# Kernel tuning notes

Measured on AMD Instinct MI355X. Metric: run time of the kernel, lower is better.

The kernel has to match this reference:

```python
import jax, jax.numpy as jnp
import numpy as np

B, N, D = 8, 4096, 512      # batch, bag_size, model dim (in_dim == att_dim)
H, DH = 8, 64               # heads, dim_head
M = 256                     # landmarks (N % M == 0 -> no padding branch)
PINV_ITERS = 6
CONV_K = 33                 # residual depthwise conv kernel (lucidrains default)


def layernorm(x, g, b, eps=1e-5):
    mu = x.mean(-1, keepdims=True)
    var = ((x - mu) ** 2).mean(-1, keepdims=True)
    return (x - mu) * jax.lax.rsqrt(var + eps) * g + b


def moore_penrose_pinv(x, iters):
    # iterative Newton-Schulz pseudo-inverse, global max normalization as in lucidrains
    abs_x = jnp.abs(x)
    col = abs_x.sum(-1)
    row = abs_x.sum(-2)
    z = jnp.swapaxes(x, -1, -2) / (jnp.max(col) * jnp.max(row))
    I = jnp.eye(x.shape[-1], dtype=x.dtype)
    for _ in range(iters):
        xz = x @ z
        z = 0.25 * z @ (13.0 * I - xz @ (15.0 * I - xz @ (7.0 * I - xz)))
    return z


def setup_inputs() -> dict:
    key = jax.random.key(0)
    ks = jax.random.split(key, 12)
    s = 0.02
    return {
        "X": jax.random.normal(ks[0], (B, N, D), dtype=jnp.float32),
        "Wqkv": jax.random.normal(ks[1], (D, 3 * H * DH), dtype=jnp.float32) * s,
        "Wout": jax.random.normal(ks[2], (H * DH, D), dtype=jnp.float32) * s,
        "bout": jnp.zeros((D,), dtype=jnp.float32),
        "conv_w": jax.random.normal(ks[3], (H, 1, CONV_K, 1), dtype=jnp.float32) * s,
        "g1": jnp.ones((D,), dtype=jnp.float32),
        "beta1": jnp.zeros((D,), dtype=jnp.float32),
        "g2": jnp.ones((D,), dtype=jnp.float32),
        "beta2": jnp.zeros((D,), dtype=jnp.float32),
        "W1": jax.random.normal(ks[4], (D, 4 * D), dtype=jnp.float32) * s,
        "b1": jnp.zeros((4 * D,), dtype=jnp.float32),
        "W2": jax.random.normal(ks[5], (4 * D, D), dtype=jnp.float32) * s,
        "b2": jnp.zeros((D,), dtype=jnp.float32),
    }


def nystrom_attention(x, Wqkv, Wout, bout, conv_w):
    b, n, _ = x.shape
    qkv = x @ Wqkv                                   # (b, n, 3*H*DH)
    qkv = qkv.reshape(b, n, 3, H, DH)
    q = jnp.transpose(qkv[:, :, 0], (0, 2, 1, 3))    # (b, H, n, DH)
    k = jnp.transpose(qkv[:, :, 1], (0, 2, 1, 3))
    v = jnp.transpose(qkv[:, :, 2], (0, 2, 1, 3))
    q = q * (DH ** -0.5)

    l = n // M  # group size per landmark
    q_l = q.reshape(b, H, M, l, DH).mean(axis=3)     # (b, H, M, DH)
    k_l = k.reshape(b, H, M, l, DH).mean(axis=3)

    sim1 = jnp.einsum("bhnd,bhmd->bhnm", q, k_l)     # (b, H, n, M)
    sim2 = jnp.einsum("bhmd,bhld->bhml", q_l, k_l)   # (b, H, M, M)
    sim3 = jnp.einsum("bhmd,bhnd->bhmn", q_l, k)     # (b, H, M, n)

    attn1 = jax.nn.softmax(sim1, axis=-1)
    attn2 = jax.nn.softmax(sim2, axis=-1)
    attn3 = jax.nn.softmax(sim3, axis=-1)

    attn2_inv = moore_penrose_pinv(attn2, PINV_ITERS)
    out = (attn1 @ attn2_inv) @ (attn3 @ v)          # (b, H, n, DH)

    # residual depthwise conv over sequence dim, heads as channels
    res = jax.lax.conv_general_dilated(
        v, conv_w, window_strides=(1, 1),
        padding=((CONV_K // 2, CONV_K // 2), (0, 0)),
        dimension_numbers=("NCHW", "OIHW", "NCHW"),
        feature_group_count=H,
    )
    out = out + res

    out = jnp.transpose(out, (0, 2, 1, 3)).reshape(b, n, H * DH)
    return out @ Wout + bout


def reference(X, Wqkv, Wout, bout, conv_w, g1, beta1, g2, beta2, W1, b1, W2, b2):
    h = layernorm(X, g1, beta1)
    h = nystrom_attention(h, Wqkv, Wout, bout, conv_w)
    # MLP with residual (use_mlp=True); dropout=0.0 -> identity
    m = layernorm(h, g2, beta2)
    m = jax.nn.gelu(m @ W1 + b1, approximate=False) @ W2 + b2
    h = h + m
    # proj_out is Identity since out_dim == att_dim
    return h
```

## Files before the change

### kernel.cpp

```cpp
#include <hip/hip_runtime.h>
#include <hip/hip_bf16.h>
#include <cmath>

#define DEV __device__ __forceinline__

namespace {

constexpr int kB = 8, kN = 4096, kD = 512, kH = 8, kDH = 64, kM = 256, kL = 16, kCK = 33;
constexpr int kBN = kB * kN;
constexpr int kBH = kB * kH;
constexpr int kHD = kH * kDH;
constexpr int kD4 = 4 * kD;
constexpr int kQKVC = 3 * kHD;

typedef __attribute__((ext_vector_type(8))) short short8;
typedef __attribute__((ext_vector_type(4))) float f32x4;

DEV float toF(float x) { return x; }
DEV float toF(__hip_bfloat16 x) { return __bfloat162float(x); }
DEV __hip_bfloat16 f2b(float f) { return __float2bfloat16(f); }
DEV short f2s(float f) {
  __hip_bfloat16 h = __float2bfloat16(f);
  return *reinterpret_cast<short*>(&h);
}
DEV float us2f(unsigned short u) { return __uint_as_float((unsigned)u << 16); }
DEV unsigned short f2us(float f) {
  __hip_bfloat16 h = __float2bfloat16(f);
  return *reinterpret_cast<unsigned short*>(&h);
}
DEV float lo16(unsigned u) { return __uint_as_float(u << 16); }
DEV float hi16(unsigned u) { return __uint_as_float(u & 0xffff0000u); }

DEV float waveSum(float v) {
#pragma unroll
  for (int o = 32; o > 0; o >>= 1) v += __shfl_down(v, o, 64);
  return v;
}
DEV float waveMax(float v) {
#pragma unroll
  for (int o = 32; o > 0; o >>= 1) v = fmaxf(v, __shfl_down(v, o, 64));
  return v;
}
DEV float blockSum(float v, float* sb) {
  v = waveSum(v);
  int lane = threadIdx.x & 63, w = threadIdx.x >> 6;
  __syncthreads();
  if (lane == 0) sb[w] = v;
  __syncthreads();
  return sb[0] + sb[1] + sb[2] + sb[3];
}
DEV float blockMax(float v, float* sb) {
  v = waveMax(v);
  int lane = threadIdx.x & 63, w = threadIdx.x >> 6;
  __syncthreads();
  if (lane == 0) sb[w] = v;
  __syncthreads();
  return fmaxf(fmaxf(sb[0], sb[1]), fmaxf(sb[2], sb[3]));
}

__global__ __launch_bounds__(256) void detect_k(const unsigned* __restrict__ x,
                                                int* __restrict__ flag) {
  __shared__ int sc[4];
  int t = threadIdx.x;
  int cb = 0;
  for (int i = t; i < 4096; i += 256) {
    unsigned w = x[i];
    float b0 = __uint_as_float(w << 16);
    float b1 = __uint_as_float(w & 0xffff0000u);
    if (fabsf(b0) < 64.0f && (b0 == 0.0f || fabsf(b0) > 1e-20f)) cb++;
    if (fabsf(b1) < 64.0f && (b1 == 0.0f || fabsf(b1) > 1e-20f)) cb++;
  }
#pragma unroll
  for (int o = 32; o > 0; o >>= 1) cb += __shfl_down(cb, o, 64);
  if ((t & 63) == 0) sc[t >> 6] = cb;
  __syncthreads();
  if (t == 0) flag[0] = (sc[0] + sc[1] + sc[2] + sc[3] > 7373) ? 1 : 0;
}

__global__ void cvt_any_k(const void* __restrict__ s, float* __restrict__ d, int n,
                          const int* __restrict__ flag) {
  int i = blockIdx.x * 256 + threadIdx.x;
  if (i >= n) return;
  if (*flag)
    d[i] = toF(((const __hip_bfloat16*)s)[i]);
  else
    d[i] = ((const float*)s)[i];
}

__global__ void cvtT_k(const void* __restrict__ s, __hip_bfloat16* __restrict__ d, int K, int N,
                       const int* __restrict__ flag) {
  int i = blockIdx.x * 256 + threadIdx.x;
  if (i >= N * K) return;
  int n = i / K, k = i - n * K;
  float v = (*flag) ? toF(((const __hip_bfloat16*)s)[(long)k * N + n])
                    : ((const float*)s)[(long)k * N + n];
  d[i] = f2b(v);
}

__global__ void f32tob16_k(const float* __restrict__ s, __hip_bfloat16* __restrict__ d, int n) {
  int i = blockIdx.x * 256 + threadIdx.x;
  if (i < n) d[i] = f2b(s[i]);
}


__global__ __launch_bounds__(256) void ln1_k(const void* __restrict__ xv,
                                             const float* __restrict__ g,
                                             const float* __restrict__ be,
                                             __hip_bfloat16* __restrict__ o,
                                             const int* __restrict__ flag) {
  __shared__ float sb[4];
  size_t row = blockIdx.x;
  __hip_bfloat16* po = o + row * kD;
  int t = threadIdx.x;
  float v0, v1;
  if (*flag) {
    const __hip_bfloat16* pr = (const __hip_bfloat16*)xv + row * kD;
    v0 = toF(pr[t]);
    v1 = toF(pr[t + 256]);
  } else {
    const float* pr = (const float*)xv + row * kD;
    v0 = pr[t];
    v1 = pr[t + 256];
  }
  float s = blockSum(v0 + v1, sb);
  float ss = blockSum(v0 * v0 + v1 * v1, sb);
  float mu = s * (1.0f / kD);
  float var = ss * (1.0f / kD) - mu * mu;
  float rs = rsqrtf(var + 1e-5f);
  po[t] = f2b((v0 - mu) * rs * g[t] + be[t]);
  po[t + 256] = f2b((v1 - mu) * rs * g[t + 256] + be[t + 256]);
}

__global__ __launch_bounds__(256) void ln2stats_k(const float* __restrict__ x,
                                                  float* __restrict__ st) {
  __shared__ float sb[4];
  size_t row = blockIdx.x;
  const float* pr = x + row * kD;
  int t = threadIdx.x;
  float v0 = pr[t], v1 = pr[t + 256];
  float s = blockSum(v0 + v1, sb);
  float ss = blockSum(v0 * v0 + v1 * v1, sb);
  if (t == 0) {
    float mu = s * (1.0f / kD);
    float var = ss * (1.0f / kD) - mu * mu;
    st[2 * row] = mu;
    st[2 * row + 1] = rsqrtf(var + 1e-5f);
  }
}


__global__ void landmark_k(const __hip_bfloat16* __restrict__ src, float* __restrict__ dst) {
  int i = blockIdx.x * 256 + threadIdx.x;
  if (i >= kBH * kM * kDH) return;
  int dh = i & 63, m = (i >> 6) & 255, bh = i >> 14;
  const __hip_bfloat16* p = src + ((size_t)bh * kN + m * kL) * kDH + dh;
  float s = 0.f;
#pragma unroll
  for (int l = 0; l < kL; ++l) s += toF(p[l * kDH]);
  dst[i] = s * (1.0f / kL);
}

__global__ __launch_bounds__(256) void softmax_k(float* __restrict__ X, int ncols) {
  __shared__ float sb[4];
  size_t row = blockIdx.x;
  float* p = X + row * ncols;
  int t = threadIdx.x;
  float mx = -1e30f;
  for (int c = t; c < ncols; c += 256) mx = fmaxf(mx, p[c]);
  mx = blockMax(mx, sb);
  float s = 0.f;
  for (int c = t; c < ncols; c += 256) {
    float e = expf(fminf(p[c] - mx, 0.0f));
    p[c] = e;
    s += e;
  }
  s = blockSum(s, sb);
  float inv = 1.0f / s;
  for (int c = t; c < ncols; c += 256) p[c] *= inv;
}

__global__ __launch_bounds__(256) void pinv_rowcol_k(const float* __restrict__ a2,
                                                     float* __restrict__ rsum,
                                                     float* __restrict__ csum) {
  __shared__ float sb[4];
  int bh = blockIdx.x >> 8, i = blockIdx.x & 255;
  const float* base = a2 + ((size_t)bh << 16);
  int t = threadIdx.x;
  float rs = blockSum(fabsf(base[i * kM + t]), sb);
  float cs = blockSum(fabsf(base[t * kM + i]), sb);
  if (t == 0) {
    rsum[blockIdx.x] = rs;
    csum[blockIdx.x] = cs;
  }
}

__global__ __launch_bounds__(256) void pinv_gmax_k(const float* __restrict__ rsum,
                                                   const float* __restrict__ csum,
                                                   float* __restrict__ gmax) {
  __shared__ float sb[4];
  int t = threadIdx.x;
  float a = 0.f, b = 0.f;
  for (int j = t; j < kBH * kM; j += 256) {
    a = fmaxf(a, rsum[j]);
    b = fmaxf(b, csum[j]);
  }
  a = blockMax(a, sb);
  b = blockMax(b, sb);
  if (t == 0) {
    gmax[0] = a;
    gmax[1] = b;
  }
}

__global__ void pinv_init_k(const float* __restrict__ a2, const float* __restrict__ gmax,
                            __hip_bfloat16* __restrict__ z) {
  int i = blockIdx.x * 256 + threadIdx.x;
  if (i >= kBH * kM * kM) return;
  int col = i & 255, r = (i >> 8) & 255, bh = i >> 16;
  float denom = fmaxf(gmax[0] * gmax[1], 1e-30f);
  z[i] = f2b(a2[((size_t)bh << 16) + col * kM + r] / denom);
}

constexpr int kCR = 128;
constexpr int kCHA = kCK / 2;
constexpr int kCW = kCR + 2 * kCHA;
constexpr int kCP = 72;

__global__ __launch_bounds__(256) void conv_add2_k(const __hip_bfloat16* __restrict__ v,
                                                   const float* __restrict__ w,
                                                   __hip_bfloat16* __restrict__ ao) {
  __shared__ short Vt[kCW * kCP];
  __shared__ float wsh[kCK];
  const int t = threadIdx.x;
  const int bh = blockIdx.x >> 5;
  const int n0 = (blockIdx.x & 31) * kCR;
  const int b = bh >> 3, h = bh & 7;
  if (t < kCK) wsh[t] = w[h * kCK + t];
  const __hip_bfloat16* vbase = v + (size_t)bh * kN * kDH;
#pragma unroll
  for (int u = 0; u < (kCW * 8 + 255) / 256; ++u) {
    const int idx = u * 256 + t;
    if (idx < kCW * 8) {
      const int r = idx >> 3, c8 = (idx & 7) * 8;
      const int n = n0 - kCHA + r;
      uint4 d = {0u, 0u, 0u, 0u};
      if (n >= 0 && n < kN) d = *(const uint4*)(vbase + (size_t)n * kDH + c8);
      *(uint4*)&Vt[r * kCP + c8] = d;
    }
  }
  __syncthreads();
  const int dh8 = (t & 7) * 8;
  const int rg = (t >> 3) * 4;
  float acc[4][8] = {};
#pragma unroll
  for (int wd = 0; wd < kCK + 3; ++wd) {
    short8 v8 = *(const short8*)&Vt[(rg + wd) * kCP + dh8];
    float f[8];
#pragma unroll
    for (int e = 0; e < 8; ++e) f[e] = us2f((unsigned short)v8[e]);
#pragma unroll
    for (int i = 0; i < 4; ++i) {
      const int tap = wd - i;
      if (tap >= 0 && tap < kCK) {
        const float wt = wsh[tap];
#pragma unroll
        for (int e = 0; e < 8; ++e) acc[i][e] = fmaf(f[e], wt, acc[i][e]);
      }
    }
  }
#pragma unroll
  for (int i = 0; i < 4; ++i) {
    const int n = n0 + rg + i;
    __hip_bfloat16* ap = ao + ((size_t)(b * kN + n)) * kHD + h * kDH + dh8;
    uint4 d = *(const uint4*)ap;
    const unsigned short* us = (const unsigned short*)&d;
    unsigned short ov[8];
#pragma unroll
    for (int e = 0; e < 8; ++e) ov[e] = f2us(us2f(us[e]) + acc[i][e]);
    *(uint4*)ap = *(const uint4*)ov;
  }
}

constexpr int FP = 72;

template <bool A3>
__global__ __launch_bounds__(256, 1) void fattn_k(const void* __restrict__ Qp,
                                                  const void* __restrict__ Kp,
                                                  const void* __restrict__ Vp,
                                                  void* __restrict__ Op) {
  __shared__ __align__(16) char smem[111616];
  short* Ks = (short*)smem;
  short* Vs = (short*)(smem + 36864);
  short* Ps = (short*)(smem + 73728);
  float* wred = (float*)(smem + 110592);
  float* Comb = (float*)smem;

  const int t = threadIdx.x;
  const int lane = t & 63, wave = t >> 6;
  const int l15 = lane & 15, quad = lane >> 4;
  const int bh = A3 ? (blockIdx.x >> 2) : (blockIdx.x >> 6);
  const int q0 = A3 ? ((blockIdx.x & 3) * 64) : ((blockIdx.x & 63) * 64);
  const int NTILES = A3 ? (kN / 256) : 1;
  short* Psw = Ps + wave * 64 * FP;

  short8 aq[4][2];
#pragma unroll
  for (int i = 0; i < 4; ++i) {
    const long qrow = (A3 ? ((long)bh * kM) : ((long)bh * kN)) + q0 + i * 16 + l15;
#pragma unroll
    for (int s = 0; s < 2; ++s) {
      if constexpr (A3) {
        const f32x4* p = (const f32x4*)((const float*)Qp + qrow * kDH + quad * 8 + s * 32);
        f32x4 a = p[0], b = p[1];
        short8 v;
#pragma unroll
        for (int e = 0; e < 4; ++e) { v[e] = f2s(a[e]); v[4 + e] = f2s(b[e]); }
        aq[i][s] = v;
      } else {
        aq[i][s] =
            *(const short8*)((const __hip_bfloat16*)Qp + qrow * kDH + quad * 8 + s * 32);
      }
    }
  }

  f32x4 o[4][4] = {};
  float mrow[4][4], lrow[4][4];
#pragma unroll
  for (int i = 0; i < 4; ++i)
#pragma unroll
    for (int rg = 0; rg < 4; ++rg) {
      mrow[i][rg] = -1e30f;
      lrow[i][rg] = 0.f;
    }

  const long kvbase = (long)bh * (A3 ? kN : kM) * kDH;

  for (int tile = 0; tile < NTILES; ++tile) {
    {
      const int r = t >> 2, c = (t & 3) * 16;
#pragma unroll
      for (int p = 0; p < 4; ++p) {
        const int rr = p * 64 + r;
        const long src = kvbase + (long)(tile * 256 + rr) * kDH + c;
        if constexpr (A3) {
          const uint4* ks = (const uint4*)((const __hip_bfloat16*)Kp + src);
          const uint4* vs = (const uint4*)((const __hip_bfloat16*)Vp + src);
          *(uint4*)&Ks[rr * FP + c] = ks[0];
          *(uint4*)&Ks[rr * FP + c + 8] = ks[1];
          *(uint4*)&Vs[rr * FP + c] = vs[0];
          *(uint4*)&Vs[rr * FP + c + 8] = vs[1];
        } else {
          const f32x4* ks = (const f32x4*)((const float*)Kp + src);
          const f32x4* vs = (const f32x4*)((const float*)Vp + src);
          f32x4 k0 = ks[0], k1 = ks[1], k2 = ks[2], k3 = ks[3];
          f32x4 v0 = vs[0], v1 = vs[1], v2 = vs[2], v3 = vs[3];
          short8 ka, kb, va, vb;
#pragma unroll
          for (int e = 0; e < 4; ++e) {
            ka[e] = f2s(k0[e]); ka[4 + e] = f2s(k1[e]);
            kb[e] = f2s(k2[e]); kb[4 + e] = f2s(k3[e]);
            va[e] = f2s(v0[e]); va[4 + e] = f2s(v1[e]);
            vb[e] = f2s(v2[e]); vb[4 + e] = f2s(v3[e]);
          }
          *(short8*)&Ks[rr * FP + c] = ka;
          *(short8*)&Ks[rr * FP + c + 8] = kb;
          *(short8*)&Vs[rr * FP + c] = va;
          *(short8*)&Vs[rr * FP + c + 8] = vb;
        }
      }
    }
    __syncthreads();

    f32x4 sacc[4][4] = {};
#pragma unroll
    for (int s = 0; s < 2; ++s) {
      short8 bk[4];
#pragma unroll
      for (int j = 0; j < 4; ++j)
        bk[j] = *(const short8*)&Ks[(wave * 64 + j * 16 + l15) * FP + quad * 8 + s * 32];
#pragma unroll
      for (int i = 0; i < 4; ++i)
#pragma unroll
        for (int j = 0; j < 4; ++j)
          sacc[i][j] =
              __builtin_amdgcn_mfma_f32_16x16x32_bf16(aq[i][s], bk[j], sacc[i][j], 0, 0, 0);
    }

    float pmax[4][4];
#pragma unroll
    for (int i = 0; i < 4; ++i)
#pragma unroll
      for (int rg = 0; rg < 4; ++rg) {
        float v = fmaxf(fmaxf(sacc[i][0][rg], sacc[i][1][rg]),
                        fmaxf(sacc[i][2][rg], sacc[i][3][rg]));
#pragma unroll
        for (int d = 1; d < 16; d <<= 1) v = fmaxf(v, __shfl_xor(v, d, 64));
        pmax[i][rg] = v;
      }
    if (l15 == 0) {
#pragma unroll
      for (int i = 0; i < 4; ++i)
#pragma unroll
        for (int rg = 0; rg < 4; ++rg)
          wred[wave * 64 + i * 16 + quad * 4 + rg] = pmax[i][rg];
    }
    __syncthreads();

#pragma unroll
    for (int i = 0; i < 4; ++i)
#pragma unroll
      for (int rg = 0; rg < 4; ++rg) {
        const int row = i * 16 + quad * 4 + rg;
        float tm =
            fmaxf(fmaxf(wred[row], wred[64 + row]), fmaxf(wred[128 + row], wred[192 + row]));
        float mn = fmaxf(mrow[i][rg], tm);
        float c = expf(mrow[i][rg] - mn);
        mrow[i][rg] = mn;
        lrow[i][rg] *= c;
#pragma unroll
        for (int j = 0; j < 4; ++j) o[i][j][rg] *= c;
      }
#pragma unroll
    for (int i = 0; i < 4; ++i)
#pragma unroll
      for (int rg = 0; rg < 4; ++rg) {
        float ls = 0.f;
#pragma unroll
        for (int j = 0; j < 4; ++j) {
          float e = expf(sacc[i][j][rg] - mrow[i][rg]);
          ls += e;
          Psw[(i * 16 + quad * 4 + rg) * FP + j * 16 + l15] = f2s(e);
        }
#pragma unroll
        for (int d = 1; d < 16; d <<= 1) ls += __shfl_xor(ls, d, 64);
        lrow[i][rg] += ls;
      }

#pragma unroll
    for (int s = 0; s < 2; ++s) {
      short8 ap[4];
#pragma unroll
      for (int i = 0; i < 4; ++i)
        ap[i] = *(const short8*)&Psw[(i * 16 + l15) * FP + quad * 8 + s * 32];
      short8 bv[4];
#pragma unroll
      for (int j = 0; j < 4; ++j)
#pragma unroll
        for (int e = 0; e < 8; ++e)
          bv[j][e] = Vs[(wave * 64 + s * 32 + quad * 8 + e) * FP + j * 16 + l15];
#pragma unroll
      for (int i = 0; i < 4; ++i)
#pragma unroll
        for (int j = 0; j < 4; ++j)
          o[i][j] = __builtin_amdgcn_mfma_f32_16x16x32_bf16(ap[i], bv[j], o[i][j], 0, 0, 0);
    }
    __syncthreads();
  }

#pragma unroll
  for (int i = 0; i < 4; ++i)
#pragma unroll
    for (int j = 0; j < 4; ++j)
#pragma unroll
      for (int rg = 0; rg < 4; ++rg)
        Comb[wave * 4096 + (i * 16 + quad * 4 + rg) * 64 + j * 16 + l15] = o[i][j][rg];
  if (l15 == 0) {
#pragma unroll
    for (int i = 0; i < 4; ++i)
#pragma unroll
      for (int rg = 0; rg < 4; ++rg)
        wred[wave * 64 + i * 16 + quad * 4 + rg] = lrow[i][rg];
  }
  __syncthreads();
#pragma unroll
  for (int u = 0; u < 16; ++u) {
    const int idx = u * 256 + t;
    const int row = idx >> 6, dh = idx & 63;
    float v = Comb[idx] + Comb[4096 + idx] + Comb[8192 + idx] + Comb[12288 + idx];
    float linv = 1.0f / (wred[row] + wred[64 + row] + wred[128 + row] + wred[192 + row]);
    if constexpr (A3) {
      ((float*)Op)[((size_t)bh * kM + q0 + row) * kDH + dh] = v * linv;
    } else {
      const int b = bh >> 3, h = bh & 7;
      ((__hip_bfloat16*)Op)[((size_t)(b * kN + q0 + row)) * kHD + h * kDH + dh] =
          f2b(v * linv);
    }
  }
}

constexpr int EPI_F32 = 0, EPI_QKV = 1, EPI_BIAS_F32 = 2, EPI_GELU_BF16 = 3, EPI_RES_OUT = 4,
              EPI_BF16 = 5;

struct EpiArgs {
  const float* bias;
  const float* res;
  __hip_bfloat16* oq;
  __hip_bfloat16* ok;
  __hip_bfloat16* ov;
  __hip_bfloat16* obf;
  const float* stats;
  const float* g;
  const float* be;
  void* ovoid;
  const int* flag;
  float eyeC;
  float eyeS;
};

template <int EPI, bool TRB, bool BEYE, bool LNA, class TAT>
__global__ __launch_bounds__(256) void mgemm_k(const TAT* __restrict__ A, int lda, long sA,
                                               const __hip_bfloat16* __restrict__ B, int ldb,
                                               long sB, float* __restrict__ C, int ldc, long sC,
                                               int K, EpiArgs ep) {
  __shared__ short As[128 * 40];
  __shared__ short Bs[128 * 40];
  A += (long)blockIdx.z * sA;
  B += (long)blockIdx.z * sB;
  const long cbase = (long)blockIdx.z * sC;
  const int row0 = blockIdx.x * 128, col0 = blockIdx.y * 128;
  const int t = threadIdx.x;
  const int lane = t & 63, wave = t >> 6;
  const int wr = (wave >> 1) * 64, wc = (wave & 1) * 64;
  const int l15 = lane & 15, quad = lane >> 4;
  f32x4 acc[4][4] = {};
  for (int k0 = 0; k0 < K; k0 += 32) {
    {
      const int kc = (t & 3) * 8;
#pragma unroll
      for (int p = 0; p < 2; ++p) {
        const int m = p * 64 + (t >> 2);
        const long r = row0 + m;
        if constexpr (LNA) {
          const float* ap = (const float*)A + r * lda + k0 + kc;
          float mu = ep.stats[2 * r], rs = ep.stats[2 * r + 1];
          short8 vv;
#pragma unroll
          for (int e = 0; e < 8; ++e)
            vv[e] = f2s((ap[e] - mu) * rs * ep.g[k0 + kc + e] + ep.be[k0 + kc + e]);
          *(short8*)(&As[m * 40 + kc]) = vv;
        } else {
          uint4 u = *(const uint4*)((const __hip_bfloat16*)A + r * lda + k0 + kc);
          *(uint4*)(&As[m * 40 + kc]) = u;
        }
      }
    }
    if (TRB) {
      const int kc = (t & 3) * 8;
#pragma unroll
      for (int p = 0; p < 2; ++p) {
        const int n = p * 64 + (t >> 2);
        uint4 u = *(const uint4*)(B + (long)(col0 + n) * ldb + k0 + kc);
        *(uint4*)(&Bs[n * 40 + kc]) = u;
      }
    } else {
      const int k8 = (t & 3) * 8;
#pragma unroll
      for (int p = 0; p < 2; ++p) {
        const int n = p * 64 + (t >> 2);
        short8 vv;
#pragma unroll
        for (int e = 0; e < 8; ++e) {
          float v = toF(B[(long)(k0 + k8 + e) * ldb + col0 + n]);
          if constexpr (BEYE) v = (((k0 + k8 + e) == (col0 + n)) ? ep.eyeC : 0.0f) - v;
          vv[e] = f2s(BEYE ? v * ep.eyeS : v);
        }
        *(short8*)(&Bs[n * 40 + k8]) = vv;
      }
    }
    __syncthreads();
    short8 af[4], bf[4];
#pragma unroll
    for (int i = 0; i < 4; ++i)
      af[i] = *(const short8*)(&As[(wr + i * 16 + l15) * 40 + quad * 8]);
#pragma unroll
    for (int j = 0; j < 4; ++j)
      bf[j] = *(const short8*)(&Bs[(wc + j * 16 + l15) * 40 + quad * 8]);
#pragma unroll
    for (int i = 0; i < 4; ++i)
#pragma unroll
      for (int j = 0; j < 4; ++j)
        acc[i][j] = __builtin_amdgcn_mfma_f32_16x16x32_bf16(af[i], bf[j], acc[i][j], 0, 0, 0);
    __syncthreads();
  }
#pragma unroll
  for (int i = 0; i < 4; ++i) {
#pragma unroll
    for (int j = 0; j < 4; ++j) {
#pragma unroll
      for (int rg = 0; rg < 4; ++rg) {
        int r = row0 + wr + i * 16 + quad * 4 + rg;
        int c = col0 + wc + j * 16 + l15;
        float v = acc[i][j][rg];
        if (EPI == EPI_BF16) {
          ep.obf[cbase + (long)r * ldc + c] = f2b(v);
        } else if (EPI == EPI_QKV) {
          int three = c >> 9, h = (c >> 6) & 7, dh = c & 63;
          int b = r >> 12, n = r & (kN - 1);
          long dst = ((long)(b * kH + h) * kN + n) * kDH + dh;
          if (three == 0)
            ep.oq[dst] = f2b(v * 0.125f);
          else if (three == 1)
            ep.ok[dst] = f2b(v);
          else
            ep.ov[dst] = f2b(v);
        } else if (EPI == EPI_BIAS_F32) {
          C[cbase + (long)r * ldc + c] = v + ep.bias[c];
        } else if (EPI == EPI_GELU_BF16) {
          v += ep.bias[c];
          ep.obf[cbase + (long)r * ldc + c] =
              f2b(0.5f * v * (1.0f + erff(v * 0.70710678118654752f)));
        } else if (EPI == EPI_RES_OUT) {
          long idx = cbase + (long)r * ldc + c;
          float v2 = v + ep.bias[c] + ep.res[idx];
          if (!(v2 == v2)) v2 = 0.0f;
          if (*ep.flag)
            ((__hip_bfloat16*)ep.ovoid)[idx] = f2b(v2);
          else
            ((float*)ep.ovoid)[idx] = v2;
        }
      }
    }
  }
}

template <int EPI, bool TRB, class TAT, class TBT>
__global__ __launch_bounds__(256) void gemm_k(const TAT* __restrict__ A, int lda, long sA,
                                              const TBT* __restrict__ B, int ldb, long sB,
                                              float* __restrict__ C, int ldc, long sC, int K,
                                              EpiArgs ep) {
  __shared__ float As[16][68];
  __shared__ float Bs[16][68];
  A += (long)blockIdx.z * sA;
  B += (long)blockIdx.z * sB;
  const long cbase = (long)blockIdx.z * sC;
  const int row0 = blockIdx.x * 64, col0 = blockIdx.y * 64;
  const int t = threadIdx.x;
  const int ty = t >> 4, tx = t & 15;
  float acc[4][4] = {{0.f, 0.f, 0.f, 0.f}, {0.f, 0.f, 0.f, 0.f},
                     {0.f, 0.f, 0.f, 0.f}, {0.f, 0.f, 0.f, 0.f}};
  const int ka = t & 15, ra = t >> 4;
  for (int k0 = 0; k0 < K; k0 += 16) {
#pragma unroll
    for (int j = 0; j < 4; ++j)
      As[ka][ra + 16 * j] = toF(A[(long)(row0 + ra + 16 * j) * lda + (k0 + ka)]);
    if (TRB) {
#pragma unroll
      for (int j = 0; j < 4; ++j)
        Bs[ka][ra + 16 * j] = toF(B[(long)(col0 + ra + 16 * j) * ldb + (k0 + ka)]);
    } else {
      const int jb = t & 63, kb = t >> 6;
#pragma unroll
      for (int j = 0; j < 4; ++j)
        Bs[kb + 4 * j][jb] = toF(B[(long)(k0 + kb + 4 * j) * ldb + (col0 + jb)]);
    }
    __syncthreads();
#pragma unroll
    for (int kk = 0; kk < 16; ++kk) {
      float av[4], bv[4];
#pragma unroll
      for (int i = 0; i < 4; ++i) av[i] = As[kk][ty * 4 + i];
#pragma unroll
      for (int j = 0; j < 4; ++j) bv[j] = Bs[kk][tx * 4 + j];
#pragma unroll
      for (int i = 0; i < 4; ++i)
#pragma unroll
        for (int j = 0; j < 4; ++j) acc[i][j] += av[i] * bv[j];
    }
    __syncthreads();
  }
#pragma unroll
  for (int i = 0; i < 4; ++i) {
    int r = row0 + ty * 4 + i;
#pragma unroll
    for (int j = 0; j < 4; ++j) {
      int c = col0 + tx * 4 + j;
      C[cbase + (long)r * ldc + c] = acc[i][j];
    }
  }
}

}

extern "C" void kernel_launch(void* const* d_in, const int* in_sizes, int n_in, void* d_out,
                              int out_size, void* d_ws, size_t ws_size, hipStream_t stream) {
  (void)in_sizes; (void)n_in; (void)out_size;

  char* base = (char*)d_ws;
  size_t off = 0;
  auto alloc = [&](size_t bytes) {
    char* p = base + off;
    off = (off + bytes + 255) & ~(size_t)255;
    return p;
  };
  float* a2 = (float*)alloc((size_t)kBH * kM * kM * 4);
  __hip_bfloat16* zs0 = (__hip_bfloat16*)alloc((size_t)kBH * kM * kM * 4);
  __hip_bfloat16* zs1 = (__hip_bfloat16*)alloc((size_t)kBH * kM * kM * 4);
  __hip_bfloat16* zs2 = (__hip_bfloat16*)alloc((size_t)kBH * kM * kM * 4);
  __hip_bfloat16* zs3 = (__hip_bfloat16*)alloc((size_t)kBH * kM * kM * 4);
  __hip_bfloat16* a2b = (__hip_bfloat16*)alloc((size_t)kBH * kM * kM * 2);
  __hip_bfloat16* q = (__hip_bfloat16*)alloc((size_t)kBH * kN * kDH * 2);
  __hip_bfloat16* kk = (__hip_bfloat16*)alloc((size_t)kBH * kN * kDH * 2);
  __hip_bfloat16* vv = (__hip_bfloat16*)alloc((size_t)kBH * kN * kDH * 2);
  __hip_bfloat16* ao = (__hip_bfloat16*)alloc((size_t)kBN * kHD * 2);
  float* ql = (float*)alloc((size_t)kBH * kM * kDH * 4);
  float* kl = (float*)alloc((size_t)kBH * kM * kDH * 4);
  float* w3 = (float*)alloc((size_t)kBH * kM * kDH * 4);
  float* y = (float*)alloc((size_t)kBH * kM * kDH * 4);
  float* st2 = (float*)alloc((size_t)kBN * 2 * 4);
  float* rsum = (float*)alloc((size_t)kBH * kM * 4);
  float* csum = (float*)alloc((size_t)kBH * kM * 4);
  float* gmax = (float*)alloc(256);
  int* dflag = (int*)alloc(256);
  __hip_bfloat16* WqkvT = (__hip_bfloat16*)alloc((size_t)kQKVC * kD * 2);
  __hip_bfloat16* WoutT = (__hip_bfloat16*)alloc((size_t)kD * kHD * 2);
  __hip_bfloat16* W1T = (__hip_bfloat16*)alloc((size_t)kD4 * kD * 2);
  __hip_bfloat16* W2T = (__hip_bfloat16*)alloc((size_t)kD * kD4 * 2);
  float* bout_f = (float*)alloc(kD * 4);
  float* b1_f = (float*)alloc(kD4 * 4);
  float* b2_f = (float*)alloc(kD * 4);
  float* convw_f = (float*)alloc(kH * kCK * 4);
  float* g1_f = (float*)alloc(kD * 4);
  float* be1_f = (float*)alloc(kD * 4);
  float* g2_f = (float*)alloc(kD * 4);
  float* be2_f = (float*)alloc(kD * 4);
  __hip_bfloat16* hln = (__hip_bfloat16*)a2;
  float* hbuf = a2;
  __hip_bfloat16* hidden = q;

  if (off > ws_size) return;

  detect_k<<<1, 256, 0, stream>>>((const unsigned*)d_in[0], dflag);

  auto cvt = [&](const void* src, float* dst, int n) {
    cvt_any_k<<<(n + 255) / 256, 256, 0, stream>>>(src, dst, n, dflag);
  };
  cvtT_k<<<(kD * kQKVC + 255) / 256, 256, 0, stream>>>(d_in[1], WqkvT, kD, kQKVC, dflag);
  cvtT_k<<<(kHD * kD + 255) / 256, 256, 0, stream>>>(d_in[2], WoutT, kHD, kD, dflag);
  cvtT_k<<<(kD * kD4 + 255) / 256, 256, 0, stream>>>(d_in[9], W1T, kD, kD4, dflag);
  cvtT_k<<<(kD4 * kD + 255) / 256, 256, 0, stream>>>(d_in[11], W2T, kD4, kD, dflag);
  cvt(d_in[3], bout_f, kD);
  cvt(d_in[4], convw_f, kH * kCK);
  cvt(d_in[5], g1_f, kD);
  cvt(d_in[6], be1_f, kD);
  cvt(d_in[7], g2_f, kD);
  cvt(d_in[8], be2_f, kD);
  cvt(d_in[10], b1_f, kD4);
  cvt(d_in[12], b2_f, kD);

  EpiArgs e0 = {};

  ln1_k<<<kBN, 256, 0, stream>>>(d_in[0], g1_f, be1_f, hln, dflag);

  EpiArgs eq = {};
  eq.oq = q; eq.ok = kk; eq.ov = vv;
  mgemm_k<EPI_QKV, true, false, false, __hip_bfloat16>
      <<<dim3(kBN / 128, kQKVC / 128, 1), 256, 0, stream>>>(hln, kD, 0, WqkvT, kD, 0, nullptr, 0,
                                                            0, kD, eq);

  landmark_k<<<(kBH * kM * kDH + 255) / 256, 256, 0, stream>>>(q, ql);
  landmark_k<<<(kBH * kM * kDH + 255) / 256, 256, 0, stream>>>(kk, kl);

  const long sQL = (long)kM * kDH, sA2 = (long)kM * kM;

  gemm_k<EPI_F32, true, float, float><<<dim3(kM / 64, kM / 64, kBH), 256, 0, stream>>>(
      ql, kDH, sQL, kl, kDH, sQL, a2, kM, sA2, kDH, e0);
  softmax_k<<<kBH * kM, 256, 0, stream>>>(a2, kM);

  f32tob16_k<<<(kBH * kM * kM + 255) / 256, 256, 0, stream>>>(a2, a2b, kBH * kM * kM);
  pinv_rowcol_k<<<kBH * kM, 256, 0, stream>>>(a2, rsum, csum);
  pinv_gmax_k<<<1, 256, 0, stream>>>(rsum, csum, gmax);
  pinv_init_k<<<(kBH * kM * kM + 255) / 256, 256, 0, stream>>>(a2, gmax, zs0);

  __hip_bfloat16* bufs[4] = {zs0, zs1, zs2, zs3};
  int zi = 0;
  dim3 gP(kM / 128, kM / 128, kBH);
  for (int it = 0; it < 6; ++it) {
    int o0 = (zi + 1) & 3, o1 = (zi + 2) & 3, o2 = (zi + 3) & 3;
    __hip_bfloat16* Z = bufs[zi];
    __hip_bfloat16* T1 = bufs[o0];
    __hip_bfloat16* T3 = bufs[o1];
    __hip_bfloat16* P3 = bufs[o2];
    EpiArgs ep1 = {}; ep1.obf = T1;
    mgemm_k<EPI_BF16, false, false, false, __hip_bfloat16><<<gP, 256, 0, stream>>>(
        a2b, kM, sA2, Z, kM, sA2, nullptr, kM, sA2, kM, ep1);
    EpiArgs ep2 = {}; ep2.obf = T3; ep2.eyeC = 7.0f; ep2.eyeS = 1.0f;
    mgemm_k<EPI_BF16, false, true, false, __hip_bfloat16><<<gP, 256, 0, stream>>>(
        T1, kM, sA2, T1, kM, sA2, nullptr, kM, sA2, kM, ep2);
    EpiArgs ep3 = {}; ep3.obf = P3; ep3.eyeC = 15.0f; ep3.eyeS = 1.0f;
    mgemm_k<EPI_BF16, false, true, false, __hip_bfloat16><<<gP, 256, 0, stream>>>(
        T1, kM, sA2, T3, kM, sA2, nullptr, kM, sA2, kM, ep3);
    EpiArgs ep4 = {}; ep4.obf = T3; ep4.eyeC = 13.0f; ep4.eyeS = 0.25f;
    mgemm_k<EPI_BF16, false, true, false, __hip_bfloat16><<<gP, 256, 0, stream>>>(
        Z, kM, sA2, P3, kM, sA2, nullptr, kM, sA2, kM, ep4);
    zi = o1;
  }
  __hip_bfloat16* zfin = bufs[zi];

  fattn_k<true><<<kBH * (kM / 64), 256, 0, stream>>>(ql, kk, vv, w3);

  gemm_k<EPI_F32, false, __hip_bfloat16, float><<<dim3(kM / 64, 1, kBH), 256, 0, stream>>>(
      zfin, kM, sA2, w3, kDH, sQL, y, kDH, sQL, kM, e0);

  fattn_k<false><<<kBH * (kN / 64), 256, 0, stream>>>(q, kl, y, ao);

  conv_add2_k<<<kBH * (kN / kCR), 256, 0, stream>>>(vv, convw_f, ao);

  EpiArgs ew = {}; ew.bias = bout_f;
  mgemm_k<EPI_BIAS_F32, true, false, false, __hip_bfloat16>
      <<<dim3(kBN / 128, kD / 128, 1), 256, 0, stream>>>(ao, kHD, 0, WoutT, kHD, 0, hbuf, kD, 0,
                                                         kHD, ew);

  ln2stats_k<<<kBN, 256, 0, stream>>>(hbuf, st2);
  EpiArgs e1 = {}; e1.bias = b1_f; e1.stats = st2; e1.g = g2_f; e1.be = be2_f; e1.obf = hidden;
  mgemm_k<EPI_GELU_BF16, true, false, true, float>
      <<<dim3(kBN / 128, kD4 / 128, 1), 256, 0, stream>>>(hbuf, kD, 0, W1T, kD, 0, nullptr, kD4,
                                                          0, kD, e1);

  EpiArgs e2 = {}; e2.bias = b2_f; e2.res = hbuf; e2.ovoid = d_out; e2.flag = dflag;
  mgemm_k<EPI_RES_OUT, true, false, false, __hip_bfloat16>
      <<<dim3(kBN / 128, kD / 128, 1), 256, 0, stream>>>(hidden, kD4, 0, W2T, kD4, 0, nullptr,
                                                         kD, 0, kD4, e2);
}
```

Measured before the change: 1.604 ms.

## Use direct global-to-LDS loads in mgemm and pre-convert attention operands to bf16

The mgemm tile loads now use global_load_lds to copy A and transposed-B tiles straight into LDS with an unpadded 32-element stride. This removes the register round trip for those loads. The fused LayerNorm-on-A path is replaced by a standalone ln2 kernel that writes bf16 activations into the output buffer. The fp32 landmark and intermediate tensors (ql, kl, y) are converted to bf16 by separate kernels, so fattn_k becomes bf16-only. The trade-off is extra launches and memory traffic, plus possible LDS bank conflicts from dropping the padding.

```diff
diff --git a/kernel.cpp b/kernel.cpp
--- a/kernel.cpp
+++ b/kernel.cpp
@@ -28,8 +28,12 @@
   __hip_bfloat16 h = __float2bfloat16(f);
   return *reinterpret_cast<unsigned short*>(&h);
 }
-DEV float lo16(unsigned u) { return __uint_as_float(u << 16); }
-DEV float hi16(unsigned u) { return __uint_as_float(u & 0xffff0000u); }
+
+DEV void gload16(const void* g, void* l) {
+  __builtin_amdgcn_global_load_lds(
+      (const __attribute__((address_space(1))) unsigned*)g,
+      (__attribute__((address_space(3))) unsigned*)l, 16, 0, 0);
+}
 
 DEV float waveSum(float v) {
 #pragma unroll
@@ -131,21 +135,23 @@
   po[t + 256] = f2b((v1 - mu) * rs * g[t + 256] + be[t + 256]);
 }
 
-__global__ __launch_bounds__(256) void ln2stats_k(const float* __restrict__ x,
-                                                  float* __restrict__ st) {
+__global__ __launch_bounds__(256) void ln2_k(const float* __restrict__ x,
+                                             const float* __restrict__ g,
+                                             const float* __restrict__ be,
+                                             __hip_bfloat16* __restrict__ o) {
   __shared__ float sb[4];
   size_t row = blockIdx.x;
   const float* pr = x + row * kD;
+  __hip_bfloat16* po = o + row * kD;
   int t = threadIdx.x;
   float v0 = pr[t], v1 = pr[t + 256];
   float s = blockSum(v0 + v1, sb);
   float ss = blockSum(v0 * v0 + v1 * v1, sb);
-  if (t == 0) {
-    float mu = s * (1.0f / kD);
-    float var = ss * (1.0f / kD) - mu * mu;
-    st[2 * row] = mu;
-    st[2 * row + 1] = rsqrtf(var + 1e-5f);
-  }
+  float mu = s * (1.0f / kD);
+  float var = ss * (1.0f / kD) - mu * mu;
+  float rs = rsqrtf(var + 1e-5f);
+  po[t] = f2b((v0 - mu) * rs * g[t] + be[t]);
+  po[t + 256] = f2b((v1 - mu) * rs * g[t + 256] + be[t + 256]);
 }
 
 
@@ -284,9 +290,9 @@
 constexpr int FP = 72;
 
 template <bool A3>
-__global__ __launch_bounds__(256, 1) void fattn_k(const void* __restrict__ Qp,
-                                                  const void* __restrict__ Kp,
-                                                  const void* __restrict__ Vp,
+__global__ __launch_bounds__(256, 1) void fattn_k(const __hip_bfloat16* __restrict__ Qp,
+                                                  const __hip_bfloat16* __restrict__ Kp,
+                                                  const __hip_bfloat16* __restrict__ Vp,
                                                   void* __restrict__ Op) {
   __shared__ __align__(16) char smem[111616];
   short* Ks = (short*)smem;
@@ -308,19 +314,8 @@
   for (int i = 0; i < 4; ++i) {
     const long qrow = (A3 ? ((long)bh * kM) : ((long)bh * kN)) + q0 + i * 16 + l15;
 #pragma unroll
-    for (int s = 0; s < 2; ++s) {
-      if constexpr (A3) {
-        const f32x4* p = (const f32x4*)((const float*)Qp + qrow * kDH + quad * 8 + s * 32);
-        f32x4 a = p[0], b = p[1];
-        short8 v;
-#pragma unroll
-        for (int e = 0; e < 4; ++e) { v[e] = f2s(a[e]); v[4 + e] = f2s(b[e]); }
-        aq[i][s] = v;
-      } else {
-        aq[i][s] =
-            *(const short8*)((const __hip_bfloat16*)Qp + qrow * kDH + quad * 8 + s * 32);
-      }
-    }
+    for (int s = 0; s < 2; ++s)
+      aq[i][s] = *(const short8*)(Qp + qrow * kDH + quad * 8 + s * 32);
   }
 
   f32x4 o[4][4] = {};
@@ -342,31 +337,12 @@
       for (int p = 0; p < 4; ++p) {
         const int rr = p * 64 + r;
         const long src = kvbase + (long)(tile * 256 + rr) * kDH + c;
-        if constexpr (A3) {
-          const uint4* ks = (const uint4*)((const __hip_bfloat16*)Kp + src);
-          const uint4* vs = (const uint4*)((const __hip_bfloat16*)Vp + src);
-          *(uint4*)&Ks[rr * FP + c] = ks[0];
-          *(uint4*)&Ks[rr * FP + c + 8] = ks[1];
-          *(uint4*)&Vs[rr * FP + c] = vs[0];
-          *(uint4*)&Vs[rr * FP + c + 8] = vs[1];
-        } else {
-          const f32x4* ks = (const f32x4*)((const float*)Kp + src);
-          const f32x4* vs = (const f32x4*)((const float*)Vp + src);
-          f32x4 k0 = ks[0], k1 = ks[1], k2 = ks[2], k3 = ks[3];
-          f32x4 v0 = vs[0], v1 = vs[1], v2 = vs[2], v3 = vs[3];
-          short8 ka, kb, va, vb;
-#pragma unroll
-          for (int e = 0; e < 4; ++e) {
-            ka[e] = f2s(k0[e]); ka[4 + e] = f2s(k1[e]);
-            kb[e] = f2s(k2[e]); kb[4 + e] = f2s(k3[e]);
-            va[e] = f2s(v0[e]); va[4 + e] = f2s(v1[e]);
-            vb[e] = f2s(v2[e]); vb[4 + e] = f2s(v3[e]);
-          }
-          *(short8*)&Ks[rr * FP + c] = ka;
-          *(short8*)&Ks[rr * FP + c + 8] = kb;
-          *(short8*)&Vs[rr * FP + c] = va;
-          *(short8*)&Vs[rr * FP + c + 8] = vb;
-        }
+        const uint4* ks = (const uint4*)(Kp + src);
+        const uint4* vs = (const uint4*)(Vp + src);
+        *(uint4*)&Ks[rr * FP + c] = ks[0];
+        *(uint4*)&Ks[rr * FP + c + 8] = ks[1];
+        *(uint4*)&Vs[rr * FP + c] = vs[0];
+        *(uint4*)&Vs[rr * FP + c + 8] = vs[1];
       }
     }
     __syncthreads();
@@ -498,21 +474,20 @@
   __hip_bfloat16* ok;
   __hip_bfloat16* ov;
   __hip_bfloat16* obf;
-  const float* stats;
-  const float* g;
-  const float* be;
   void* ovoid;
   const int* flag;
   float eyeC;
   float eyeS;
 };
 
-template <int EPI, bool TRB, bool BEYE, bool LNA, class TAT>
-__global__ __launch_bounds__(256) void mgemm_k(const TAT* __restrict__ A, int lda, long sA,
-                                               const __hip_bfloat16* __restrict__ B, int ldb,
-                                               long sB, float* __restrict__ C, int ldc, long sC,
-                                               int K, EpiArgs ep) {
-  __shared__ short As[128 * 40];
+template <int EPI, bool TRB, bool BEYE>
+__global__ __launch_bounds__(256) void mgemm_k(const __hip_bfloat16* __restrict__ A, int lda,
+                                               long sA, const __hip_bfloat16* __restrict__ B,
+                                               int ldb, long sB, float* __restrict__ C, int ldc,
+                                               long sC, int K, EpiArgs ep) {
+  constexpr int LSA = 32;
+  constexpr int LSB = TRB ? 32 : 40;
+  __shared__ short As[128 * 32];
   __shared__ short Bs[128 * 40];
   A += (long)blockIdx.z * sA;
   B += (long)blockIdx.z * sB;
@@ -529,19 +504,7 @@
 #pragma unroll
       for (int p = 0; p < 2; ++p) {
         const int m = p * 64 + (t >> 2);
-        const long r = row0 + m;
-        if constexpr (LNA) {
-          const float* ap = (const float*)A + r * lda + k0 + kc;
-          float mu = ep.stats[2 * r], rs = ep.stats[2 * r + 1];
-          short8 vv;
-#pragma unroll
-          for (int e = 0; e < 8; ++e)
-            vv[e] = f2s((ap[e] - mu) * rs * ep.g[k0 + kc + e] + ep.be[k0 + kc + e]);
-          *(short8*)(&As[m * 40 + kc]) = vv;
-        } else {
-          uint4 u = *(const uint4*)((const __hip_bfloat16*)A + r * lda + k0 + kc);
-          *(uint4*)(&As[m * 40 + kc]) = u;
-        }
+        gload16(A + (long)(row0 + m) * lda + k0 + kc, &As[p * 2048 + t * 8]);
       }
     }
     if (TRB) {
@@ -549,8 +512,7 @@
 #pragma unroll
       for (int p = 0; p < 2; ++p) {
         const int n = p * 64 + (t >> 2);
-        uint4 u = *(const uint4*)(B + (long)(col0 + n) * ldb + k0 + kc);
-        *(uint4*)(&Bs[n * 40 + kc]) = u;
+        gload16(B + (long)(col0 + n) * ldb + k0 + kc, &Bs[p * 2048 + t * 8]);
       }
     } else {
       const int k8 = (t & 3) * 8;
@@ -564,17 +526,17 @@
           if constexpr (BEYE) v = (((k0 + k8 + e) == (col0 + n)) ? ep.eyeC : 0.0f) - v;
           vv[e] = f2s(BEYE ? v * ep.eyeS : v);
         }
-        *(short8*)(&Bs[n * 40 + k8]) = vv;
+        *(short8*)(&Bs[n * LSB + k8]) = vv;
       }
     }
     __syncthreads();
     short8 af[4], bf[4];
 #pragma unroll
     for (int i = 0; i < 4; ++i)
-      af[i] = *(const short8*)(&As[(wr + i * 16 + l15) * 40 + quad * 8]);
+      af[i] = *(const short8*)(&As[(wr + i * 16 + l15) * LSA + quad * 8]);
 #pragma unroll
     for (int j = 0; j < 4; ++j)
-      bf[j] = *(const short8*)(&Bs[(wc + j * 16 + l15) * 40 + quad * 8]);
+      bf[j] = *(const short8*)(&Bs[(wc + j * 16 + l15) * LSB + quad * 8]);
 #pragma unroll
     for (int i = 0; i < 4; ++i)
 #pragma unroll
@@ -706,7 +668,6 @@
   float* kl = (float*)alloc((size_t)kBH * kM * kDH * 4);
   float* w3 = (float*)alloc((size_t)kBH * kM * kDH * 4);
   float* y = (float*)alloc((size_t)kBH * kM * kDH * 4);
-  float* st2 = (float*)alloc((size_t)kBN * 2 * 4);
   float* rsum = (float*)alloc((size_t)kBH * kM * 4);
   float* csum = (float*)alloc((size_t)kBH * kM * 4);
   float* gmax = (float*)alloc(256);
@@ -726,6 +687,10 @@
   __hip_bfloat16* hln = (__hip_bfloat16*)a2;
   float* hbuf = a2;
   __hip_bfloat16* hidden = q;
+  __hip_bfloat16* qlb = a2b;
+  __hip_bfloat16* klb = a2b + (size_t)kBH * kM * kDH;
+  __hip_bfloat16* ylb = a2b + 2 * (size_t)kBH * kM * kDH;
+  __hip_bfloat16* hln2 = (__hip_bfloat16*)d_out;
 
   if (off > ws_size) return;
 
@@ -753,7 +718,7 @@
 
   EpiArgs eq = {};
   eq.oq = q; eq.ok = kk; eq.ov = vv;
-  mgemm_k<EPI_QKV, true, false, false, __hip_bfloat16>
+  mgemm_k<EPI_QKV, true, false>
       <<<dim3(kBN / 128, kQKVC / 128, 1), 256, 0, stream>>>(hln, kD, 0, WqkvT, kD, 0, nullptr, 0,
                                                             0, kD, eq);
 
@@ -781,43 +746,47 @@
     __hip_bfloat16* T3 = bufs[o1];
     __hip_bfloat16* P3 = bufs[o2];
     EpiArgs ep1 = {}; ep1.obf = T1;
-    mgemm_k<EPI_BF16, false, false, false, __hip_bfloat16><<<gP, 256, 0, stream>>>(
+    mgemm_k<EPI_BF16, false, false><<<gP, 256, 0, stream>>>(
         a2b, kM, sA2, Z, kM, sA2, nullptr, kM, sA2, kM, ep1);
     EpiArgs ep2 = {}; ep2.obf = T3; ep2.eyeC = 7.0f; ep2.eyeS = 1.0f;
-    mgemm_k<EPI_BF16, false, true, false, __hip_bfloat16><<<gP, 256, 0, stream>>>(
+    mgemm_k<EPI_BF16, false, true><<<gP, 256, 0, stream>>>(
         T1, kM, sA2, T1, kM, sA2, nullptr, kM, sA2, kM, ep2);
     EpiArgs ep3 = {}; ep3.obf = P3; ep3.eyeC = 15.0f; ep3.eyeS = 1.0f;
-    mgemm_k<EPI_BF16, false, true, false, __hip_bfloat16><<<gP, 256, 0, stream>>>(
+    mgemm_k<EPI_BF16, false, true><<<gP, 256, 0, stream>>>(
         T1, kM, sA2, T3, kM, sA2, nullptr, kM, sA2, kM, ep3);
     EpiArgs ep4 = {}; ep4.obf = T3; ep4.eyeC = 13.0f; ep4.eyeS = 0.25f;
-    mgemm_k<EPI_BF16, false, true, false, __hip_bfloat16><<<gP, 256, 0, stream>>>(
+    mgemm_k<EPI_BF16, false, true><<<gP, 256, 0, stream>>>(
         Z, kM, sA2, P3, kM, sA2, nullptr, kM, sA2, kM, ep4);
     zi = o1;
   }
   __hip_bfloat16* zfin = bufs[zi];
 
-  fattn_k<true><<<kBH * (kM / 64), 256, 0, stream>>>(ql, kk, vv, w3);
+  f32tob16_k<<<(kBH * kM * kDH + 255) / 256, 256, 0, stream>>>(ql, qlb, kBH * kM * kDH);
+  f32tob16_k<<<(kBH * kM * kDH + 255) / 256, 256, 0, stream>>>(kl, klb, kBH * kM * kDH);
+
+  fattn_k<true><<<kBH * (kM / 64), 256, 0, stream>>>(qlb, kk, vv, w3);
 
   gemm_k<EPI_F32, false, __hip_bfloat16, float><<<dim3(kM / 64, 1, kBH), 256, 0, stream>>>(
       zfin, kM, sA2, w3, kDH, sQL, y, kDH, sQL, kM, e0);
-
-  fattn_k<false><<<kBH * (kN / 64), 256, 0, stream>>>(q, kl, y, ao);
+  f32tob16_k<<<(kBH * kM * kDH + 255) / 256, 256, 0, stream>>>(y, ylb, kBH * kM * kDH);
+
+  fattn_k<false><<<kBH * (kN / 64), 256, 0, stream>>>(q, klb, ylb, ao);
 
   conv_add2_k<<<kBH * (kN / kCR), 256, 0, stream>>>(vv, convw_f, ao);
 
   EpiArgs ew = {}; ew.bias = bout_f;
-  mgemm_k<EPI_BIAS_F32, true, false, false, __hip_bfloat16>
+  mgemm_k<EPI_BIAS_F32, true, false>
       <<<dim3(kBN / 128, kD / 128, 1), 256, 0, stream>>>(ao, kHD, 0, WoutT, kHD, 0, hbuf, kD, 0,
                                                          kHD, ew);
 
-  ln2stats_k<<<kBN, 256, 0, stream>>>(hbuf, st2);
-  EpiArgs e1 = {}; e1.bias = b1_f; e1.stats = st2; e1.g = g2_f; e1.be = be2_f; e1.obf = hidden;
-  mgemm_k<EPI_GELU_BF16, true, false, true, float>
-      <<<dim3(kBN / 128, kD4 / 128, 1), 256, 0, stream>>>(hbuf, kD, 0, W1T, kD, 0, nullptr, kD4,
+  ln2_k<<<kBN, 256, 0, stream>>>(hbuf, g2_f, be2_f, hln2);
+  EpiArgs e1 = {}; e1.bias = b1_f; e1.obf = hidden;
+  mgemm_k<EPI_GELU_BF16, true, false>
+      <<<dim3(kBN / 128, kD4 / 128, 1), 256, 0, stream>>>(hln2, kD, 0, W1T, kD, 0, nullptr, kD4,
                                                           0, kD, e1);
 
   EpiArgs e2 = {}; e2.bias = b2_f; e2.res = hbuf; e2.ovoid = d_out; e2.flag = dflag;
-  mgemm_k<EPI_RES_OUT, true, false, false, __hip_bfloat16>
+  mgemm_k<EPI_RES_OUT, true, false>
       <<<dim3(kBN / 128, kD / 128, 1), 256, 0, stream>>>(hidden, kD4, 0, W2T, kD4, 0, nullptr,
                                                          kD, 0, kD4, e2);
 }
```

Result: no change. 1.587 ms (-1.0%).
